# Kernel optimization log

Hardware: AMD Instinct MI355X
Metric: run time of the kernel (lower is better)

## Reference

```python
import jax, jax.numpy as jnp
import numpy as np

EMBED, HID, H = 1024, 1024, 16
D = HID // H
B, L = 4, 4096


def setup_inputs() -> dict:
    key = jax.random.key(0)
    ks = jax.random.split(key, 16)
    s = 0.02
    return {
        "emb": jax.random.normal(ks[0], (B, L, EMBED), jnp.float32),
        "Wa_w": jax.random.normal(ks[1], (HID, EMBED), jnp.float32) * s,
        "Wa_b": jnp.zeros((HID,), jnp.float32),
        "Wb_w": jax.random.normal(ks[2], (HID, EMBED), jnp.float32) * s,
        "Wb_b": jnp.zeros((HID,), jnp.float32),
        "Wo_w": jax.random.normal(ks[3], (HID, EMBED), jnp.float32) * s,
        "Wo_b": jnp.zeros((HID,), jnp.float32),
        "C_w": jax.random.normal(ks[4], (HID, HID), jnp.float32) * s,
        "C_b": jnp.zeros((HID,), jnp.float32),
        "ln_g": jnp.ones((HID,), jnp.float32),
        "ln_b": jnp.zeros((HID,), jnp.float32),
        "f1_w": jax.random.normal(ks[5], (4 * HID, HID), jnp.float32) * s,
        "f1_b": jnp.zeros((4 * HID,), jnp.float32),
        "f2_w": jax.random.normal(ks[6], (HID, 4 * HID), jnp.float32) * s,
        "f2_b": jnp.zeros((HID,), jnp.float32),
        "p_w": jax.random.normal(ks[7], (HID, HID), jnp.float32) * s,
        "p_b": jnp.zeros((HID,), jnp.float32),
        "head_weights": jnp.ones((H,), jnp.float32),
    }


def _layernorm(x, g, b, eps=1e-5):
    mu = jnp.mean(x, axis=-1, keepdims=True)
    var = jnp.mean(jnp.square(x - mu), axis=-1, keepdims=True)
    return (x - mu) * jax.lax.rsqrt(var + eps) * g + b


def _affine_combine(x, y):
    a1, b1 = x
    a2, b2 = y
    return a1 * a2, a2 * b1 + b2


def reference(emb, Wa_w, Wa_b, Wb_w, Wb_b, Wo_w, Wo_b, C_w, C_b, ln_g, ln_b,
              f1_w, f1_b, f2_w, f2_b, p_w, p_b, head_weights):
    Bv, Lv, _ = emb.shape
    a = jnp.tanh(emb @ Wa_w.T + Wa_b).reshape(Bv, Lv, H, D)
    b = (emb @ Wb_w.T + Wb_b).reshape(Bv, Lv, H, D)
    w = (emb @ Wo_w.T + Wo_b).reshape(Bv, Lv, H, D)
    # h_t = a_t * h_{t-1} + b_t, h_0 = 0 -> parallel associative scan over L
    _, h_seq = jax.lax.associative_scan(_affine_combine, (a, b), axis=1)
    # batched per-step C projection over full hidden dim
    c_out = (h_seq.reshape(Bv, Lv, HID) @ C_w.T + C_b).reshape(Bv, Lv, H, D)
    z = (head_weights[None, None, :, None] * (c_out + w)).reshape(Bv, Lv, HID)
    u = z + _layernorm(z, ln_g, ln_b)
    ffn = jax.nn.gelu(u @ f1_w.T + f1_b, approximate=False)
    out = ffn @ f2_w.T + f2_b
    return (u + out) @ p_w.T + p_b
```

## Files before the change

### kernel.cpp

```cpp
#include <hip/hip_runtime.h>
#include <hip/hip_bf16.h>

typedef __attribute__((ext_vector_type(8))) short short8;
typedef __attribute__((ext_vector_type(4))) float f32x4;

#define DEVI static __device__ __forceinline__

constexpr int HID = 1024;
constexpr int BB = 4, LL = 4096;
constexpr int MROWS = BB * LL;
constexpr int NCH = 64, TCH = 64;

constexpr size_t ELN_EMB  = 0;
constexpr size_t ELN_WABO = 16777216;
constexpr size_t ELN_CW   = 19922944;
constexpr size_t ELN_F1   = 20971520;
constexpr size_t ELN_F2   = 25165824;
constexpr size_t ELN_PW   = 29360128;
constexpr size_t ELN_END  = 30408704;
constexpr size_t POOL_BYTES = ELN_END * 2;

constexpr size_t OFF_ABW = POOL_BYTES;
constexpr size_t OFF_H   = OFF_ABW + (size_t)MROWS*3072*2;
constexpr size_t OFF_U   = OFF_H  + (size_t)MROWS*1024*2;
constexpr size_t OFF_AGG = OFF_U  + (size_t)MROWS*1024*2;
constexpr size_t AG_ELEMS = (size_t)BB * NCH * HID;
constexpr size_t WS_NEEDED = OFF_AGG + AG_ELEMS * 4 * 3;

DEVI unsigned short f2b(float x) {
  unsigned u = __float_as_uint(x);
  return (unsigned short)((u + 0x7fffu + ((u >> 16) & 1u)) >> 16);
}
DEVI float b2f(unsigned short u) { return __uint_as_float((unsigned)u << 16); }

DEVI float fast_tanh(float y) {
  y = fminf(fmaxf(y, -10.f), 10.f);
  float e = __expf(2.f * y);
  return (e - 1.f) / (e + 1.f);
}
DEVI float gelu_fast(float x) {
  float t = 0.7978845608028654f * (x + 0.044715f * x * x * x);
  return 0.5f * x * (1.f + fast_tanh(t));
}

DEVI void gload_lds16(const unsigned short* g, unsigned short* l) {
  __builtin_amdgcn_global_load_lds(
      (const __attribute__((address_space(1))) void*)g,
      (__attribute__((address_space(3))) void*)l, 16, 0, 0);
}
DEVI void sbar() { __builtin_amdgcn_s_barrier(); }

constexpr long CH_EMB = 16777216 / 8;
constexpr long CH_W   = 1048576 / 8;
constexpr long CH_F   = 4194304 / 8;
constexpr long SEG1 = CH_EMB;
constexpr long SEG2 = SEG1 + CH_W;
constexpr long SEG3 = SEG2 + CH_W;
constexpr long SEG4 = SEG3 + CH_W;
constexpr long SEG5 = SEG4 + CH_W;
constexpr long SEG6 = SEG5 + CH_F;
constexpr long SEG7 = SEG6 + CH_F;
constexpr long SEG8 = SEG7 + CH_W;

__global__ __launch_bounds__(256) void convert_all(
    const float* __restrict__ emb, const float* __restrict__ wa,
    const float* __restrict__ wb,  const float* __restrict__ wo,
    const float* __restrict__ cw,  const float* __restrict__ f1,
    const float* __restrict__ f2,  const float* __restrict__ pw,
    unsigned short* __restrict__ dst) {
  const long stride = (long)gridDim.x * blockDim.x;
  for (long ck = (long)blockIdx.x * blockDim.x + threadIdx.x; ck < SEG8; ck += stride) {
    const float* s; size_t d;
    if (ck < SEG1)      { s = emb + (size_t)ck * 8;        d = ELN_EMB + (size_t)ck * 8; }
    else if (ck < SEG2) { s = wa + (size_t)(ck-SEG1) * 8;  d = ELN_WABO + (size_t)(ck-SEG1) * 8; }
    else if (ck < SEG3) { s = wb + (size_t)(ck-SEG2) * 8;  d = ELN_WABO + 1048576 + (size_t)(ck-SEG2) * 8; }
    else if (ck < SEG4) { s = wo + (size_t)(ck-SEG3) * 8;  d = ELN_WABO + 2097152 + (size_t)(ck-SEG3) * 8; }
    else if (ck < SEG5) { s = cw + (size_t)(ck-SEG4) * 8;  d = ELN_CW + (size_t)(ck-SEG4) * 8; }
    else if (ck < SEG6) { s = f1 + (size_t)(ck-SEG5) * 8;  d = ELN_F1 + (size_t)(ck-SEG5) * 8; }
    else if (ck < SEG7) { s = f2 + (size_t)(ck-SEG6) * 8;  d = ELN_F2 + (size_t)(ck-SEG6) * 8; }
    else                { s = pw + (size_t)(ck-SEG7) * 8;  d = ELN_PW + (size_t)(ck-SEG7) * 8; }
    float4 x = *(const float4*)s;
    float4 y = *(const float4*)(s + 4);
    short8 o;
    o[0]=(short)f2b(x.x); o[1]=(short)f2b(x.y); o[2]=(short)f2b(x.z); o[3]=(short)f2b(x.w);
    o[4]=(short)f2b(y.x); o[5]=(short)f2b(y.y); o[6]=(short)f2b(y.z); o[7]=(short)f2b(y.w);
    *(short8*)(dst + d) = o;
  }
}

template <int EPI>
__global__ __launch_bounds__(512) void gemm256(
    const unsigned short* __restrict__ A, const unsigned short* __restrict__ Bw,
    int K, int NITER, int ldo, int addld,
    const float* __restrict__ biasA, const float* __restrict__ biasB,
    const float* __restrict__ biasW,
    const unsigned short* __restrict__ addB, const float* __restrict__ hw,
    float* __restrict__ outF, unsigned short* __restrict__ outB) {
  __shared__ alignas(16) unsigned short lds[2][2][16384];
  const int tid = threadIdx.x;
  const int lane = tid & 63, wave = tid >> 6;
  const int wr = wave >> 2, wc = wave & 3;
  const int arow0 = blockIdx.x * 256, bcol0 = blockIdx.y * 256;
  f32x4 acc[8][4] = {};
  const int fm = lane & 15, fg = lane >> 4;
  const int sA = (fg ^ (fm & 7)) * 8;
  const int sB = ((4 + fg) ^ (fm & 7)) * 8;
  const int NT = NITER * 2;

#define MKSRC(l)                                                                   \
  const unsigned short* src##l; {                                                  \
    const int row_ = (tid >> 3) + 64 * l;                                          \
    const int c_ = (tid & 7) ^ (row_ & 7);                                         \
    src##l = (c_ < 4) ? A + (size_t)(arow0 + row_) * K + c_ * 8                    \
                      : Bw + (size_t)(bcol0 + row_) * K + (c_ - 4) * 8; }
  MKSRC(0) MKSRC(1) MKSRC(2) MKSRC(3)
#undef MKSRC

#define STG0(bf, ks, kt) do { const int ko_ = (kt) * 64 + (ks) * 32;               \
    gload_lds16(src0 + ko_, &lds[bf][ks][tid * 8]);                                \
    gload_lds16(src1 + ko_, &lds[bf][ks][4096 + tid * 8]); } while (0)
#define STG1(bf, ks, kt) do { const int ko_ = (kt) * 64 + (ks) * 32;               \
    gload_lds16(src2 + ko_, &lds[bf][ks][8192 + tid * 8]);                         \
    gload_lds16(src3 + ko_, &lds[bf][ks][12288 + tid * 8]); } while (0)

  short8 bfr[4];
#define PHASE(BUF, KS, MH, NEWB, STG, DOVM) do {                                   \
    const unsigned short* lab = &lds[BUF][KS][0];                                  \
    if (NEWB) {                                                                    \
      _Pragma("unroll") for (int n = 0; n < 4; ++n)                                \
        bfr[n] = *(const short8*)(lab + (wc * 64 + n * 16 + fm) * 64 + sB);        \
    }                                                                              \
    short8 af[4];                                                                  \
    _Pragma("unroll") for (int m = 0; m < 4; ++m)                                  \
      af[m] = *(const short8*)(lab + (wr * 128 + MH * 64 + m * 16 + fm) * 64 + sA);\
    STG;                                                                           \
    if (DOVM) asm volatile("s_waitcnt vmcnt(8)" ::: "memory");                     \
    __builtin_amdgcn_s_barrier();                                                  \
    asm volatile("s_waitcnt lgkmcnt(0)" ::: "memory");                             \
    __builtin_amdgcn_sched_barrier(0);     \
    __builtin_amdgcn_s_setprio(1);                                                 \
    _Pragma("unroll") for (int m = 0; m < 4; ++m)                                  \
      _Pragma("unroll") for (int n = 0; n < 4; ++n)                                \
        acc[MH * 4 + m][n] = __builtin_amdgcn_mfma_f32_16x16x32_bf16(              \
            af[m], bfr[n], acc[MH * 4 + m][n], 0, 0, 0);                           \
    __builtin_amdgcn_s_setprio(0);                                                 \
    __builtin_amdgcn_s_barrier();                                                  \
    __builtin_amdgcn_sched_barrier(0);                                             \
  } while (0)

  STG0(0, 0, 0); STG1(0, 0, 0);
  STG0(0, 1, 0); STG1(0, 1, 0);
  STG0(1, 0, 1); STG1(1, 0, 1);
  asm volatile("s_waitcnt vmcnt(8)" ::: "memory");
  sbar();
  __builtin_amdgcn_sched_barrier(0);

  for (int it = 0; it < NITER; ++it) {
    const int t1 = 2 * it + 1;
    const int t2 = (2 * it + 2 < NT) ? 2 * it + 2 : 0;
    const int t3 = (2 * it + 3 < NT) ? 2 * it + 3 : 1;
    PHASE(0, 0, 0, true,  STG0(1, 1, t1), false);
    PHASE(0, 0, 1, false, STG1(1, 1, t1), true);
    PHASE(0, 1, 0, true,  STG0(0, 0, t2), false);
    PHASE(0, 1, 1, false, STG1(0, 0, t2), true);
    PHASE(1, 0, 0, true,  STG0(0, 1, t2), false);
    PHASE(1, 0, 1, false, STG1(0, 1, t2), true);
    PHASE(1, 1, 0, true,  STG0(1, 0, t3), false);
    PHASE(1, 1, 1, false, STG1(1, 0, t3), true);
  }
#undef PHASE
#undef STG0
#undef STG1

  const int crow = (lane >> 4) * 4, ccol = lane & 15;
#pragma unroll
  for (int m = 0; m < 8; ++m) {
    const int row0 = arow0 + wr * 128 + (m >> 2) * 64 + (m & 3) * 16 + crow;
#pragma unroll
    for (int n = 0; n < 4; ++n) {
      const int col = bcol0 + wc * 64 + n * 16 + ccol;
#pragma unroll
      for (int r = 0; r < 4; ++r) {
        const size_t orow = (size_t)(row0 + r);
        float x = acc[m][n][r];
        if constexpr (EPI == 0) {
          const int cb = col >> 10;
          const float* bp = (cb == 0) ? biasA : (cb == 1 ? biasB : biasW);
          x += bp[col & 1023];
          if (cb == 0) x = fast_tanh(x);
          outB[orow * 3072 + col] = f2b(x);
        } else if constexpr (EPI == 1) {
          x += biasA[col] + b2f(addB[orow * (size_t)addld + col]);
          x *= hw[col >> 6];
          outB[orow * (size_t)ldo + col] = f2b(x);
        } else if constexpr (EPI == 2) {
          x += biasA[col];
          outB[orow * (size_t)ldo + col] = f2b(gelu_fast(x));
        } else if constexpr (EPI == 3) {
          x += biasA[col] + b2f(addB[orow * (size_t)addld + col]);
          outB[orow * (size_t)ldo + col] = f2b(x);
        } else {
          outF[orow * (size_t)ldo + col] = x + biasA[col];
        }
      }
    }
  }
}

__global__ __launch_bounds__(256) void scan_p1(const unsigned short* __restrict__ abw,
                                               float* __restrict__ agA,
                                               float* __restrict__ agB) {
  const int idx = blockIdx.x;
  const int cg = idx & 3, ch = (idx >> 2) & (NCH - 1), bb = idx >> 8;
  const int c = cg * 256 + threadIdx.x;
  const size_t base = ((size_t)bb * LL + (size_t)ch * TCH) * 3072 + c;
  float A = 1.f, Bg = 0.f;
#pragma unroll 4
  for (int t = 0; t < TCH; ++t) {
    float at = b2f(abw[base + (size_t)t * 3072]);
    float bt = b2f(abw[base + (size_t)t * 3072 + 1024]);
    Bg = fmaf(at, Bg, bt);
    A *= at;
  }
  const size_t o = ((size_t)bb * NCH + ch) * HID + c;
  agA[o] = A;
  agB[o] = Bg;
}

__global__ __launch_bounds__(256) void scan_p2(const float* __restrict__ agA,
                                               const float* __restrict__ agB,
                                               float* __restrict__ pre) {
  const int gid = blockIdx.x * 256 + threadIdx.x;
  const int bb = gid >> 10, c = gid & 1023;
  float h = 0.f;
  for (int ch = 0; ch < NCH; ++ch) {
    const size_t o = ((size_t)bb * NCH + ch) * HID + c;
    pre[o] = h;
    h = fmaf(agA[o], h, agB[o]);
  }
}

__global__ __launch_bounds__(256) void scan_p3(const unsigned short* __restrict__ abw,
                                               const float* __restrict__ pre,
                                               unsigned short* __restrict__ hout) {
  const int idx = blockIdx.x;
  const int cg = idx & 3, ch = (idx >> 2) & (NCH - 1), bb = idx >> 8;
  const int c = cg * 256 + threadIdx.x;
  const size_t base = ((size_t)bb * LL + (size_t)ch * TCH) * 3072 + c;
  const size_t hbase = ((size_t)bb * LL + (size_t)ch * TCH) * HID + c;
  float h = pre[((size_t)bb * NCH + ch) * HID + c];
#pragma unroll 4
  for (int t = 0; t < TCH; ++t) {
    float at = b2f(abw[base + (size_t)t * 3072]);
    float bt = b2f(abw[base + (size_t)t * 3072 + 1024]);
    h = fmaf(at, h, bt);
    hout[hbase + (size_t)t * HID] = f2b(h);
  }
}

__global__ __launch_bounds__(256) void ln_kernel(const unsigned short* __restrict__ abw,
                                                 const float* __restrict__ gam,
                                                 const float* __restrict__ bet,
                                                 unsigned short* __restrict__ u) {
  const int wave = threadIdx.x >> 6, lane = threadIdx.x & 63;
  const int row = blockIdx.x * 4 + wave;
  const unsigned short* zr = abw + (size_t)row * 3072 + lane * 16;
  short8 z0 = *(const short8*)zr;
  short8 z1 = *(const short8*)(zr + 8);
  float x[16];
#pragma unroll
  for (int e = 0; e < 8; ++e) {
    x[e]     = b2f((unsigned short)z0[e]);
    x[8 + e] = b2f((unsigned short)z1[e]);
  }
  float s = 0.f, s2 = 0.f;
#pragma unroll
  for (int e = 0; e < 16; ++e) { s += x[e]; s2 += x[e] * x[e]; }
#pragma unroll
  for (int off = 32; off > 0; off >>= 1) {
    s += __shfl_xor(s, off, 64);
    s2 += __shfl_xor(s2, off, 64);
  }
  const float mu = s * (1.f / 1024.f);
  const float var = s2 * (1.f / 1024.f) - mu * mu;
  const float rs = rsqrtf(var + 1e-5f);
  const float* gp = gam + lane * 16;
  const float* bp = bet + lane * 16;
  short8 o0, o1;
#pragma unroll
  for (int e = 0; e < 8; ++e) {
    float v0 = x[e]     + (x[e]     - mu) * rs * gp[e]     + bp[e];
    float v1 = x[8 + e] + (x[8 + e] - mu) * rs * gp[8 + e] + bp[8 + e];
    o0[e] = (short)f2b(v0);
    o1[e] = (short)f2b(v1);
  }
  unsigned short* ur = u + (size_t)row * HID + lane * 16;
  *(short8*)ur = o0;
  *(short8*)(ur + 8) = o1;
}

extern "C" void kernel_launch(void* const* d_in, const int* in_sizes, int n_in,
                              void* d_out, int out_size, void* d_ws, size_t ws_size,
                              hipStream_t stream) {
  if (ws_size < WS_NEEDED) return;

  const float* emb   = (const float*)d_in[0];
  const float* Wa_w  = (const float*)d_in[1];
  const float* Wa_b  = (const float*)d_in[2];
  const float* Wb_w  = (const float*)d_in[3];
  const float* Wb_b  = (const float*)d_in[4];
  const float* Wo_w  = (const float*)d_in[5];
  const float* Wo_b  = (const float*)d_in[6];
  const float* C_w   = (const float*)d_in[7];
  const float* C_b   = (const float*)d_in[8];
  const float* ln_g  = (const float*)d_in[9];
  const float* ln_b  = (const float*)d_in[10];
  const float* f1_w  = (const float*)d_in[11];
  const float* f1_b  = (const float*)d_in[12];
  const float* f2_w  = (const float*)d_in[13];
  const float* f2_b  = (const float*)d_in[14];
  const float* p_w   = (const float*)d_in[15];
  const float* p_b   = (const float*)d_in[16];
  const float* headw = (const float*)d_in[17];

  char* ws = (char*)d_ws;
  unsigned short* bfp  = (unsigned short*)ws;
  unsigned short* abwB = (unsigned short*)(ws + OFF_ABW);
  unsigned short* hB   = (unsigned short*)(ws + OFF_H);
  unsigned short* uB   = (unsigned short*)(ws + OFF_U);
  unsigned short* ffnB = abwB;
  float* agA = (float*)(ws + OFF_AGG);
  float* agB = agA + AG_ELEMS;
  float* pre = agB + AG_ELEMS;

  convert_all<<<2048, 256, 0, stream>>>(emb, Wa_w, Wb_w, Wo_w, C_w, f1_w, f2_w, p_w, bfp);

  gemm256<0><<<dim3(64, 12), 512, 0, stream>>>(
      bfp + ELN_EMB, bfp + ELN_WABO, 1024, 8, 3072, 0,
      Wa_b, Wb_b, Wo_b, nullptr, nullptr, nullptr, abwB);

  scan_p1<<<BB * NCH * 4, 256, 0, stream>>>(abwB, agA, agB);
  scan_p2<<<16, 256, 0, stream>>>(agA, agB, pre);
  scan_p3<<<BB * NCH * 4, 256, 0, stream>>>(abwB, pre, hB);

  gemm256<1><<<dim3(64, 4), 512, 0, stream>>>(
      hB, bfp + ELN_CW, 1024, 8, 3072, 3072,
      C_b, nullptr, nullptr, abwB + 2048, headw, nullptr, abwB);

  ln_kernel<<<4096, 256, 0, stream>>>(abwB, ln_g, ln_b, uB);

  gemm256<2><<<dim3(64, 16), 512, 0, stream>>>(
      uB, bfp + ELN_F1, 1024, 8, 4096, 0,
      f1_b, nullptr, nullptr, nullptr, nullptr, nullptr, ffnB);

  gemm256<3><<<dim3(64, 4), 512, 0, stream>>>(
      ffnB, bfp + ELN_F2, 4096, 32, 1024, 1024,
      f2_b, nullptr, nullptr, uB, nullptr, nullptr, uB);

  gemm256<4><<<dim3(64, 4), 512, 0, stream>>>(
      uB, bfp + ELN_PW, 1024, 8, 1024, 0,
      p_b, nullptr, nullptr, nullptr, nullptr, (float*)d_out, nullptr);
}
```

Baseline: 566.3 us.

## Use 16 waves per GEMM block with 64x64 warp tiles

Doubles the GEMM block from 512 to 1024 threads (16 waves in a 4x4 arrangement). Each wave now owns a 64x64 output tile instead of 128x64, which halves accumulator registers, and each thread issues half as many staging loads. The K-loop is restructured into four phases per iteration with a single combined staging macro. The aim is more latency hiding per CU, at the cost of extra barrier participants and reloading B fragments in every phase.

```diff
diff --git a/kernel.cpp b/kernel.cpp
--- a/kernel.cpp
+++ b/kernel.cpp
@@ -89,7 +89,7 @@
 }
 
 template <int EPI>
-__global__ __launch_bounds__(512) void gemm256(
+__global__ __launch_bounds__(1024) void gemm256(
     const unsigned short* __restrict__ A, const unsigned short* __restrict__ Bw,
     int K, int NITER, int ldo, int addld,
     const float* __restrict__ biasA, const float* __restrict__ biasB,
@@ -101,7 +101,7 @@
   const int lane = tid & 63, wave = tid >> 6;
   const int wr = wave >> 2, wc = wave & 3;
   const int arow0 = blockIdx.x * 256, bcol0 = blockIdx.y * 256;
-  f32x4 acc[8][4] = {};
+  f32x4 acc[4][4] = {};
   const int fm = lane & 15, fg = lane >> 4;
   const int sA = (fg ^ (fm & 7)) * 8;
   const int sB = ((4 + fg) ^ (fm & 7)) * 8;
@@ -109,49 +109,43 @@
 
 #define MKSRC(l)                                                                   \
   const unsigned short* src##l; {                                                  \
-    const int row_ = (tid >> 3) + 64 * l;                                          \
+    const int row_ = (tid >> 3) + 128 * l;                                         \
     const int c_ = (tid & 7) ^ (row_ & 7);                                         \
     src##l = (c_ < 4) ? A + (size_t)(arow0 + row_) * K + c_ * 8                    \
                       : Bw + (size_t)(bcol0 + row_) * K + (c_ - 4) * 8; }
-  MKSRC(0) MKSRC(1) MKSRC(2) MKSRC(3)
+  MKSRC(0) MKSRC(1)
 #undef MKSRC
 
-#define STG0(bf, ks, kt) do { const int ko_ = (kt) * 64 + (ks) * 32;               \
+#define STG(bf, ks, kt) do { const int ko_ = (kt) * 64 + (ks) * 32;                \
     gload_lds16(src0 + ko_, &lds[bf][ks][tid * 8]);                                \
-    gload_lds16(src1 + ko_, &lds[bf][ks][4096 + tid * 8]); } while (0)
-#define STG1(bf, ks, kt) do { const int ko_ = (kt) * 64 + (ks) * 32;               \
-    gload_lds16(src2 + ko_, &lds[bf][ks][8192 + tid * 8]);                         \
-    gload_lds16(src3 + ko_, &lds[bf][ks][12288 + tid * 8]); } while (0)
-
-  short8 bfr[4];
-#define PHASE(BUF, KS, MH, NEWB, STG, DOVM) do {                                   \
+    gload_lds16(src1 + ko_, &lds[bf][ks][8192 + tid * 8]); } while (0)
+
+#define PHASE(BUF, KS, STGX) do {                                                  \
     const unsigned short* lab = &lds[BUF][KS][0];                                  \
-    if (NEWB) {                                                                    \
-      _Pragma("unroll") for (int n = 0; n < 4; ++n)                                \
-        bfr[n] = *(const short8*)(lab + (wc * 64 + n * 16 + fm) * 64 + sB);        \
-    }                                                                              \
-    short8 af[4];                                                                  \
+    short8 af[4], bfr[4];                                                          \
+    _Pragma("unroll") for (int n = 0; n < 4; ++n)                                  \
+      bfr[n] = *(const short8*)(lab + (wc * 64 + n * 16 + fm) * 64 + sB);          \
     _Pragma("unroll") for (int m = 0; m < 4; ++m)                                  \
-      af[m] = *(const short8*)(lab + (wr * 128 + MH * 64 + m * 16 + fm) * 64 + sA);\
-    STG;                                                                           \
-    if (DOVM) asm volatile("s_waitcnt vmcnt(8)" ::: "memory");                     \
+      af[m] = *(const short8*)(lab + (wr * 64 + m * 16 + fm) * 64 + sA);           \
+    STGX;                                                                          \
+    asm volatile("s_waitcnt vmcnt(4)" ::: "memory");                               \
     __builtin_amdgcn_s_barrier();                                                  \
     asm volatile("s_waitcnt lgkmcnt(0)" ::: "memory");                             \
-    __builtin_amdgcn_sched_barrier(0);     \
+    __builtin_amdgcn_sched_barrier(0);                                             \
     __builtin_amdgcn_s_setprio(1);                                                 \
     _Pragma("unroll") for (int m = 0; m < 4; ++m)                                  \
       _Pragma("unroll") for (int n = 0; n < 4; ++n)                                \
-        acc[MH * 4 + m][n] = __builtin_amdgcn_mfma_f32_16x16x32_bf16(              \
-            af[m], bfr[n], acc[MH * 4 + m][n], 0, 0, 0);                           \
+        acc[m][n] = __builtin_amdgcn_mfma_f32_16x16x32_bf16(                       \
+            af[m], bfr[n], acc[m][n], 0, 0, 0);                                    \
     __builtin_amdgcn_s_setprio(0);                                                 \
     __builtin_amdgcn_s_barrier();                                                  \
     __builtin_amdgcn_sched_barrier(0);                                             \
   } while (0)
 
-  STG0(0, 0, 0); STG1(0, 0, 0);
-  STG0(0, 1, 0); STG1(0, 1, 0);
-  STG0(1, 0, 1); STG1(1, 0, 1);
-  asm volatile("s_waitcnt vmcnt(8)" ::: "memory");
+  STG(0, 0, 0);
+  STG(0, 1, 0);
+  STG(1, 0, 1);
+  asm volatile("s_waitcnt vmcnt(4)" ::: "memory");
   sbar();
   __builtin_amdgcn_sched_barrier(0);
 
@@ -159,23 +153,18 @@
     const int t1 = 2 * it + 1;
     const int t2 = (2 * it + 2 < NT) ? 2 * it + 2 : 0;
     const int t3 = (2 * it + 3 < NT) ? 2 * it + 3 : 1;
-    PHASE(0, 0, 0, true,  STG0(1, 1, t1), false);
-    PHASE(0, 0, 1, false, STG1(1, 1, t1), true);
-    PHASE(0, 1, 0, true,  STG0(0, 0, t2), false);
-    PHASE(0, 1, 1, false, STG1(0, 0, t2), true);
-    PHASE(1, 0, 0, true,  STG0(0, 1, t2), false);
-    PHASE(1, 0, 1, false, STG1(0, 1, t2), true);
-    PHASE(1, 1, 0, true,  STG0(1, 0, t3), false);
-    PHASE(1, 1, 1, false, STG1(1, 0, t3), true);
+    PHASE(0, 0, STG(1, 1, t1));
+    PHASE(0, 1, STG(0, 0, t2));
+    PHASE(1, 0, STG(0, 1, t2));
+    PHASE(1, 1, STG(1, 0, t3));
   }
 #undef PHASE
-#undef STG0
-#undef STG1
+#undef STG
 
   const int crow = (lane >> 4) * 4, ccol = lane & 15;
 #pragma unroll
-  for (int m = 0; m < 8; ++m) {
-    const int row0 = arow0 + wr * 128 + (m >> 2) * 64 + (m & 3) * 16 + crow;
+  for (int m = 0; m < 4; ++m) {
+    const int row0 = arow0 + wr * 64 + m * 16 + crow;
 #pragma unroll
     for (int n = 0; n < 4; ++n) {
       const int col = bcol0 + wc * 64 + n * 16 + ccol;
@@ -335,7 +324,7 @@
 
   convert_all<<<2048, 256, 0, stream>>>(emb, Wa_w, Wb_w, Wo_w, C_w, f1_w, f2_w, p_w, bfp);
 
-  gemm256<0><<<dim3(64, 12), 512, 0, stream>>>(
+  gemm256<0><<<dim3(64, 12), 1024, 0, stream>>>(
       bfp + ELN_EMB, bfp + ELN_WABO, 1024, 8, 3072, 0,
       Wa_b, Wb_b, Wo_b, nullptr, nullptr, nullptr, abwB);
 
@@ -343,21 +332,21 @@
   scan_p2<<<16, 256, 0, stream>>>(agA, agB, pre);
   scan_p3<<<BB * NCH * 4, 256, 0, stream>>>(abwB, pre, hB);
 
-  gemm256<1><<<dim3(64, 4), 512, 0, stream>>>(
+  gemm256<1><<<dim3(64, 4), 1024, 0, stream>>>(
       hB, bfp + ELN_CW, 1024, 8, 3072, 3072,
       C_b, nullptr, nullptr, abwB + 2048, headw, nullptr, abwB);
 
   ln_kernel<<<4096, 256, 0, stream>>>(abwB, ln_g, ln_b, uB);
 
-  gemm256<2><<<dim3(64, 16), 512, 0, stream>>>(
+  gemm256<2><<<dim3(64, 16), 1024, 0, stream>>>(
       uB, bfp + ELN_F1, 1024, 8, 4096, 0,
       f1_b, nullptr, nullptr, nullptr, nullptr, nullptr, ffnB);
 
-  gemm256<3><<<dim3(64, 4), 512, 0, stream>>>(
+  gemm256<3><<<dim3(64, 4), 1024, 0, stream>>>(
       ffnB, bfp + ELN_F2, 4096, 32, 1024, 1024,
       f2_b, nullptr, nullptr, uB, nullptr, nullptr, uB);
 
-  gemm256<4><<<dim3(64, 4), 512, 0, stream>>>(
+  gemm256<4><<<dim3(64, 4), 1024, 0, stream>>>(
       uB, bfp + ELN_PW, 1024, 8, 1024, 0,
       p_b, nullptr, nullptr, nullptr, nullptr, (float*)d_out, nullptr);
 }
```

New measurement: 565.7 us. Within noise of the previous version (-0.1%).
